# Optimization experiments

Hardware: AMD Instinct MI355X
Metric: run time of the kernel (lower is better)

## Reference

```python
import jax, jax.numpy as jnp
import numpy as np

N = 98304        # total nodes (= 16384 graphs * act_dim 6)
E = 1572864      # edges (avg degree 16)
C = 64           # in_channels
H = 32           # hidden_size
ACT = 6          # act_dim


def setup_inputs() -> dict:
    key = jax.random.key(0)
    ks = jax.random.split(key, 11)
    s = lambda fan: 1.0 / np.sqrt(fan)
    return {
        "state": jax.random.normal(ks[0], (N, C), jnp.float32),
        "edge_index": jax.random.randint(ks[1], (2, E), 0, N, dtype=jnp.int64),
        "conv_W": jax.random.normal(ks[2], (C, C), jnp.float32) * s(C),
        "conv_b": jax.random.normal(ks[3], (C,), jnp.float32) * 0.01,
        "W1": jax.random.normal(ks[4], (C, H), jnp.float32) * s(C),
        "b1": jax.random.normal(ks[5], (H,), jnp.float32) * 0.01,
        "W2": jax.random.normal(ks[6], (H, H), jnp.float32) * s(H),
        "b2": jax.random.normal(ks[7], (H,), jnp.float32) * 0.01,
        "W3": jax.random.normal(ks[8], (H, 1), jnp.float32) * s(H),
        "b3": jax.random.normal(ks[9], (1,), jnp.float32) * 0.01,
    }


def gcn_conv(x, edge_index, W, b):
    # PyG GCNConv: add self-loops, symmetric normalization D^-1/2 (A+I) D^-1/2 (X W) + b
    loops = jnp.arange(N, dtype=edge_index.dtype)
    src = jnp.concatenate([edge_index[0], loops])  # [E+N]
    dst = jnp.concatenate([edge_index[1], loops])  # [E+N]
    deg = jax.ops.segment_sum(jnp.ones(E + N, x.dtype), dst, num_segments=N)
    dinv = jax.lax.rsqrt(deg)                      # deg >= 1 due to self-loops
    norm = dinv[src] * dinv[dst]                   # [E+N]
    h = x @ W                                      # [N, C]
    msg = h[src] * norm[:, None]                   # gather + scale
    return jax.ops.segment_sum(msg, dst, num_segments=N) + b


def reference(state, edge_index, conv_W, conv_b, W1, b1, W2, b2, W3, b3):
    out = jax.nn.relu(gcn_conv(state, edge_index, conv_W, conv_b))
    x = out + state                                # residual
    x = x.reshape(-1, ACT, C)                      # [num_graphs, act_dim, C]
    x = jax.nn.relu(x @ W1 + b1)
    x = jax.nn.relu(x @ W2 + b2)
    x = jax.nn.softplus(x @ W3 + b3)
    concentration = x.squeeze(-1) + 1e-20          # [num_graphs, act_dim]
    return concentration
```

## Files before the change

kernel.cpp:

```cpp
#include <hip/hip_runtime.h>
#include <math.h>

#define Nn 98304
#define Ee 1572864
#define Cc 64
#define Hh 32
#define HB 256
#define EPB (Ee / HB)
#define NST 384
#define SN 256
#define CAP_ST 4800
#define GN 64


__device__ __forceinline__ int detect64(const void* ei) {
    const unsigned int* u = (const unsigned int*)ei;
    int is64 = 1;
    #pragma unroll
    for (int i = 0; i < 16; ++i) is64 &= (u[2 * i + 1] == 0u);
    return is64;
}

__device__ __forceinline__ int load_idx(const void* ei, long e, int is64) {
    if (is64) return (int)((const long long*)ei)[e];
    return ((const int*)ei)[e];
}

__device__ __forceinline__ unsigned short f2bf(float x) {
    union { float f; unsigned int u; } v; v.f = x;
    unsigned int r = v.u + 0x7FFFu + ((v.u >> 16) & 1u);
    return (unsigned short)(r >> 16);
}
__device__ __forceinline__ float bf2f(unsigned short h) {
    union { unsigned int u; float f; } v; v.u = ((unsigned int)h) << 16;
    return v.f;
}

__global__ __launch_bounds__(1024) void k_p1(const void* __restrict__ ei,
                                             unsigned int* __restrict__ aux,
                                             unsigned int* __restrict__ ebuf) {
    __shared__ unsigned int hl[NST];
    __shared__ unsigned int cur[NST];
    int t = threadIdx.x, b = blockIdx.x;
    if (t < NST) hl[t] = 0;
    __syncthreads();
    int is64 = detect64(ei);
    long e0 = (long)b * EPB;
    #pragma unroll
    for (int i = 0; i < EPB / 1024; ++i) {
        int d = load_idx(ei, (long)Ee + e0 + i * 1024 + t, is64);
        atomicAdd(&hl[d >> 8], 1u);
    }
    __syncthreads();
    if (t < NST) cur[t] = hl[t];
    __syncthreads();
    for (int s = 1; s < NST; s <<= 1) {
        unsigned int v = (t < NST && t >= s) ? cur[t - s] : 0u;
        __syncthreads();
        if (t < NST) cur[t] += v;
        __syncthreads();
    }
    if (t < NST) {
        unsigned int ex = cur[t] - hl[t];
        aux[(long)b * NST + t] = ex | (hl[t] << 16);
        cur[t] = ex;
    }
    __syncthreads();
    #pragma unroll
    for (int i = 0; i < EPB / 1024; ++i) {
        long e = e0 + i * 1024 + t;
        int s = load_idx(ei, e, is64);
        int d = load_idx(ei, (long)Ee + e, is64);
        unsigned int pos = atomicAdd(&cur[d >> 8], 1u);
        ebuf[(long)b * EPB + pos] = (unsigned int)s | ((unsigned int)(d & (SN - 1)) << 17);
    }
}

__global__ __launch_bounds__(512) void k_p2(const unsigned int* __restrict__ aux,
                                            const unsigned int* __restrict__ ebuf,
                                            unsigned int* __restrict__ rowOff,
                                            unsigned int* __restrict__ rowEnd,
                                            float* __restrict__ dinv,
                                            unsigned int* __restrict__ srcs) {
    __shared__ unsigned int stage[CAP_ST];
    __shared__ unsigned int rbI[HB];
    __shared__ unsigned int rof[HB];
    __shared__ unsigned int cnt[SN];
    __shared__ unsigned int sc[SN];
    __shared__ unsigned int cur[SN];
    int t = threadIdx.x, st = blockIdx.x;
    if (t < HB) {
        unsigned int av = aux[(long)t * NST + st];
        rof[t] = av & 0xFFFFu;
        rbI[t] = av >> 16;
    }
    if (t < SN) cnt[t] = 0;
    __syncthreads();
    for (int s = 1; s < HB; s <<= 1) {
        unsigned int v = (t < HB && t >= s) ? rbI[t - s] : 0u;
        __syncthreads();
        if (t < HB) rbI[t] += v;
        __syncthreads();
    }
    int total = (int)rbI[HB - 1];
    for (int i = t; i < total; i += 512) {
        int lo = 0, hi = HB - 1;
        while (lo < hi) {
            int mid = (lo + hi) >> 1;
            if (rbI[mid] > (unsigned int)i) hi = mid; else lo = mid + 1;
        }
        unsigned int ex = lo ? rbI[lo - 1] : 0u;
        stage[i] = ebuf[(long)lo * EPB + rof[lo] + ((unsigned int)i - ex)];
    }
    __syncthreads();
    for (int i = t; i < total; i += 512)
        atomicAdd(&cnt[stage[i] >> 17], 1u);
    __syncthreads();
    if (t < SN) sc[t] = cnt[t];
    __syncthreads();
    #pragma unroll
    for (int off = 1; off < SN; off <<= 1) {
        unsigned int v = (t < SN && t >= off) ? sc[t - off] : 0u;
        __syncthreads();
        if (t < SN) sc[t] += v;
        __syncthreads();
    }
    if (t < SN) {
        unsigned int start = (unsigned int)(st * CAP_ST) + sc[t] - cnt[t];
        rowOff[(long)st * SN + t] = start;
        rowEnd[(long)st * SN + t] = start + cnt[t];
        cur[t] = start;
        dinv[(long)st * SN + t] = rsqrtf((float)(cnt[t] + 1));
    }
    __syncthreads();
    for (int i = t; i < total; i += 512) {
        unsigned int u = stage[i];
        unsigned int pos = atomicAdd(&cur[u >> 17], 1u);
        srcs[pos] = u & 0x1FFFFu;
    }
}

__global__ __launch_bounds__(256) void k_gemm(const float* __restrict__ state,
                                              const float* __restrict__ W,
                                              const float* __restrict__ dinv,
                                              unsigned short* __restrict__ gb) {
    __shared__ float Wl[64 * 64];
    __shared__ float Al[64 * 68];
    int t = threadIdx.x;
    long n0 = (long)blockIdx.x * 64;

    const float4* W4 = (const float4*)W;
    float4* Wl4 = (float4*)Wl;
    #pragma unroll
    for (int i = 0; i < 4; ++i) Wl4[i * 256 + t] = W4[i * 256 + t];

    const float4* S4 = (const float4*)(state) + n0 * 16;
    #pragma unroll
    for (int i = 0; i < 4; ++i) {
        int f4 = t + i * 256;
        int r = f4 >> 4, k0 = (f4 & 15) * 4;
        *(float4*)(Al + r * 68 + k0) = S4[f4];
    }
    __syncthreads();

    int r0 = (t >> 4) * 4;
    int c0 = (t & 15) * 4;
    float acc[4][4] = {{0.f}};
    #pragma unroll
    for (int kk = 0; kk < 64; kk += 4) {
        float4 a4[4], w4[4];
        #pragma unroll
        for (int i = 0; i < 4; ++i) a4[i] = *(const float4*)(Al + (r0 + i) * 68 + kk);
        #pragma unroll
        for (int j = 0; j < 4; ++j) w4[j] = *(const float4*)(Wl + (kk + j) * 64 + c0);
        const float* aa = (const float*)a4;
        const float* ww = (const float*)w4;
        #pragma unroll
        for (int i = 0; i < 4; ++i)
            #pragma unroll
            for (int j = 0; j < 4; ++j) {
                float av = aa[i * 4 + j];
                #pragma unroll
                for (int c = 0; c < 4; ++c)
                    acc[i][c] = fmaf(av, ww[j * 4 + c], acc[i][c]);
            }
    }
    #pragma unroll
    for (int i = 0; i < 4; ++i) {
        long n = n0 + r0 + i;
        float dv = dinv[n];
        ushort4 o;
        o.x = f2bf(acc[i][0] * dv); o.y = f2bf(acc[i][1] * dv);
        o.z = f2bf(acc[i][2] * dv); o.w = f2bf(acc[i][3] * dv);
        *(ushort4*)(gb + n * 64 + c0) = o;
    }
}

__global__ __launch_bounds__(512) void k_gf(const unsigned int* __restrict__ rowOff,
                                            const unsigned int* __restrict__ rowEnd,
                                            const unsigned int* __restrict__ srcs,
                                            const unsigned short* __restrict__ gb,
                                            const float* __restrict__ dinv,
                                            const float* __restrict__ state,
                                            const float* __restrict__ conv_b,
                                            const float* __restrict__ W1,
                                            const float* __restrict__ b1,
                                            const float* __restrict__ W2,
                                            const float* __restrict__ b2,
                                            const float* __restrict__ W3,
                                            const float* __restrict__ b3,
                                            float* __restrict__ out) {
    __shared__ float sa[GN * 68];
    __shared__ float hs[GN * 34];
    __shared__ float sW1[Cc * Hh];
    __shared__ float sW2[Hh * Hh];
    __shared__ float sW3[Hh], sb1[Hh], sb2[Hh], scb[Cc];
    __shared__ float sb3;
    int t = threadIdx.x;
    int wave = t >> 6, lane = t & 63;
    long n0 = (long)blockIdx.x * GN;

    for (int i = t; i < Cc * Hh; i += 512) sW1[i] = W1[i];
    for (int i = t; i < Hh * Hh; i += 512) sW2[i] = W2[i];
    if (t < Hh) { sW3[t] = W3[t]; sb1[t] = b1[t]; sb2[t] = b2[t]; }
    if (t >= 64 && t < 128) scb[t - 64] = conv_b[t - 64];
    if (t == 511) sb3 = b3[0];

    {
        int g = lane >> 3;
        int cs = lane & 7;
        int j = wave * 8 + g;
        long n = n0 + j;
        int ptr = (int)rowOff[n];
        int end = (int)rowEnd[n];
        float dv = dinv[n];
        const uint4* gb4 = (const uint4*)gb;

        float a[8];
        {
            uint4 u = gb4[n * 8 + cs];
            union { unsigned int i; float f; } w;
            w.i = u.x << 16;         a[0] = w.f;
            w.i = u.x & 0xFFFF0000u; a[1] = w.f;
            w.i = u.y << 16;         a[2] = w.f;
            w.i = u.y & 0xFFFF0000u; a[3] = w.f;
            w.i = u.z << 16;         a[4] = w.f;
            w.i = u.z & 0xFFFF0000u; a[5] = w.f;
            w.i = u.w << 16;         a[6] = w.f;
            w.i = u.w & 0xFFFF0000u; a[7] = w.f;
        }

        int cnt = end - ptr;
        while (cnt >= 4) {
            int s0 = (int)srcs[ptr];
            int s1 = (int)srcs[ptr + 1];
            int s2 = (int)srcs[ptr + 2];
            int s3 = (int)srcs[ptr + 3];
            uint4 u0 = gb4[(long)s0 * 8 + cs];
            uint4 u1 = gb4[(long)s1 * 8 + cs];
            uint4 u2 = gb4[(long)s2 * 8 + cs];
            uint4 u3 = gb4[(long)s3 * 8 + cs];
            union { unsigned int i; float f; } w;
            w.i = u0.x << 16;         a[0] += w.f;
            w.i = u0.x & 0xFFFF0000u; a[1] += w.f;
            w.i = u0.y << 16;         a[2] += w.f;
            w.i = u0.y & 0xFFFF0000u; a[3] += w.f;
            w.i = u0.z << 16;         a[4] += w.f;
            w.i = u0.z & 0xFFFF0000u; a[5] += w.f;
            w.i = u0.w << 16;         a[6] += w.f;
            w.i = u0.w & 0xFFFF0000u; a[7] += w.f;
            w.i = u1.x << 16;         a[0] += w.f;
            w.i = u1.x & 0xFFFF0000u; a[1] += w.f;
            w.i = u1.y << 16;         a[2] += w.f;
            w.i = u1.y & 0xFFFF0000u; a[3] += w.f;
            w.i = u1.z << 16;         a[4] += w.f;
            w.i = u1.z & 0xFFFF0000u; a[5] += w.f;
            w.i = u1.w << 16;         a[6] += w.f;
            w.i = u1.w & 0xFFFF0000u; a[7] += w.f;
            w.i = u2.x << 16;         a[0] += w.f;
            w.i = u2.x & 0xFFFF0000u; a[1] += w.f;
            w.i = u2.y << 16;         a[2] += w.f;
            w.i = u2.y & 0xFFFF0000u; a[3] += w.f;
            w.i = u2.z << 16;         a[4] += w.f;
            w.i = u2.z & 0xFFFF0000u; a[5] += w.f;
            w.i = u2.w << 16;         a[6] += w.f;
            w.i = u2.w & 0xFFFF0000u; a[7] += w.f;
            w.i = u3.x << 16;         a[0] += w.f;
            w.i = u3.x & 0xFFFF0000u; a[1] += w.f;
            w.i = u3.y << 16;         a[2] += w.f;
            w.i = u3.y & 0xFFFF0000u; a[3] += w.f;
            w.i = u3.z << 16;         a[4] += w.f;
            w.i = u3.z & 0xFFFF0000u; a[5] += w.f;
            w.i = u3.w << 16;         a[6] += w.f;
            w.i = u3.w & 0xFFFF0000u; a[7] += w.f;
            ptr += 4; cnt -= 4;
        }
        while (cnt > 0) {
            int s0 = (int)srcs[ptr];
            uint4 u0 = gb4[(long)s0 * 8 + cs];
            union { unsigned int i; float f; } w;
            w.i = u0.x << 16;         a[0] += w.f;
            w.i = u0.x & 0xFFFF0000u; a[1] += w.f;
            w.i = u0.y << 16;         a[2] += w.f;
            w.i = u0.y & 0xFFFF0000u; a[3] += w.f;
            w.i = u0.z << 16;         a[4] += w.f;
            w.i = u0.z & 0xFFFF0000u; a[5] += w.f;
            w.i = u0.w << 16;         a[6] += w.f;
            w.i = u0.w & 0xFFFF0000u; a[7] += w.f;
            ++ptr; --cnt;
        }

        float* r = sa + j * 68 + cs * 8;
        float4 lo, hi;
        lo.x = a[0] * dv; lo.y = a[1] * dv; lo.z = a[2] * dv; lo.w = a[3] * dv;
        hi.x = a[4] * dv; hi.y = a[5] * dv; hi.z = a[6] * dv; hi.w = a[7] * dv;
        *(float4*)r = lo;
        *(float4*)(r + 4) = hi;
    }
    __syncthreads();

    {
        int j = t >> 3, o = t & 7;
        long n = n0 + j;
        int k0 = o * 8;
        const float4* sp4 = (const float4*)(state + n * 64 + k0);
        float4 s0 = sp4[0], s1 = sp4[1];
        float* r = sa + j * 68 + k0;
        r[0] = fmaxf(r[0] + scb[k0 + 0], 0.f) + s0.x;
        r[1] = fmaxf(r[1] + scb[k0 + 1], 0.f) + s0.y;
        r[2] = fmaxf(r[2] + scb[k0 + 2], 0.f) + s0.z;
        r[3] = fmaxf(r[3] + scb[k0 + 3], 0.f) + s0.w;
        r[4] = fmaxf(r[4] + scb[k0 + 4], 0.f) + s1.x;
        r[5] = fmaxf(r[5] + scb[k0 + 5], 0.f) + s1.y;
        r[6] = fmaxf(r[6] + scb[k0 + 6], 0.f) + s1.z;
        r[7] = fmaxf(r[7] + scb[k0 + 7], 0.f) + s1.w;
    }
    __syncthreads();

    {
        int j = t >> 3, o = t & 7;
        int c0 = o * 4;
        float a0 = sb1[c0], a1 = sb1[c0 + 1], a2 = sb1[c0 + 2], a3 = sb1[c0 + 3];
        #pragma unroll
        for (int k = 0; k < Cc; ++k) {
            float xv = sa[j * 68 + k];
            float4 w = *(const float4*)(sW1 + k * Hh + c0);
            a0 = fmaf(xv, w.x, a0); a1 = fmaf(xv, w.y, a1);
            a2 = fmaf(xv, w.z, a2); a3 = fmaf(xv, w.w, a3);
        }
        float* r = hs + j * 34 + c0;
        r[0] = fmaxf(a0, 0.f); r[1] = fmaxf(a1, 0.f);
        r[2] = fmaxf(a2, 0.f); r[3] = fmaxf(a3, 0.f);
    }
    __syncthreads();

    {
        int j = t >> 3, o = t & 7;
        int c0 = o * 4;
        float a0 = sb2[c0], a1 = sb2[c0 + 1], a2 = sb2[c0 + 2], a3 = sb2[c0 + 3];
        #pragma unroll
        for (int k = 0; k < Hh; ++k) {
            float xv = hs[j * 34 + k];
            float4 w = *(const float4*)(sW2 + k * Hh + c0);
            a0 = fmaf(xv, w.x, a0); a1 = fmaf(xv, w.y, a1);
            a2 = fmaf(xv, w.z, a2); a3 = fmaf(xv, w.w, a3);
        }
        float* r = sa + j * 68 + c0;
        r[0] = fmaxf(a0, 0.f); r[1] = fmaxf(a1, 0.f);
        r[2] = fmaxf(a2, 0.f); r[3] = fmaxf(a3, 0.f);
    }
    __syncthreads();

    if (t < GN) {
        float y = sb3;
        #pragma unroll
        for (int k = 0; k < Hh; ++k) y = fmaf(sa[t * 68 + k], sW3[k], y);
        float sp = fmaxf(y, 0.f) + log1pf(expf(-fabsf(y)));
        out[n0 + t] = sp + 1e-20f;
    }
}

extern "C" void kernel_launch(void* const* d_in, const int* in_sizes, int n_in,
                              void* d_out, int out_size, void* d_ws, size_t ws_size,
                              hipStream_t stream) {
    const float* state  = (const float*)d_in[0];
    const void*  ei     = d_in[1];
    const float* conv_W = (const float*)d_in[2];
    const float* conv_b = (const float*)d_in[3];
    const float* W1 = (const float*)d_in[4];
    const float* b1 = (const float*)d_in[5];
    const float* W2 = (const float*)d_in[6];
    const float* b2 = (const float*)d_in[7];
    const float* W3 = (const float*)d_in[8];
    const float* b3 = (const float*)d_in[9];
    float* out = (float*)d_out;

    float*          dinv   = (float*)d_ws;
    unsigned short* gb     = (unsigned short*)(dinv + Nn);
    unsigned int*   rowOff = (unsigned int*)(gb + (size_t)Nn * 64);
    unsigned int*   rowEnd = rowOff + Nn;
    unsigned int*   aux    = rowEnd + Nn;
    unsigned int*   ebuf   = aux + (size_t)HB * NST;
    unsigned int*   srcs   = ebuf + Ee;

    k_p1<<<HB, 1024, 0, stream>>>(ei, aux, ebuf);
    k_p2<<<NST, 512, 0, stream>>>(aux, ebuf, rowOff, rowEnd, dinv, srcs);
    k_gemm<<<Nn / 64, 256, 0, stream>>>(state, conv_W, dinv, gb);
    k_gf<<<Nn / GN, 512, 0, stream>>>(rowOff, rowEnd, srcs, gb, dinv, state, conv_b,
                                      W1, b1, W2, b2, W3, b3, out);
}
```

Baseline: 174.5 us.

## Software-pipeline neighbor gathers and replace block barriers with wave barriers

The fused aggregation+MLP kernel now issues the next four neighbor-row gathers before accumulating the previous four, so global-load latency overlaps with the bf16 unpack-and-add work. Each wave only touches the eight nodes it owns in shared memory, so the block-wide __syncthreads between MLP stages become wave barriers, plus one block barrier after the weight staging. The final 32-wide dot product is spread across 8 lanes per node with a shuffle reduction instead of 64 serial threads. This keeps more registers live for the prefetched data, and it relies on each wave's shared-memory rows being private to that wave.

After: 172.1 us. No clear change (-1.4%).

```diff
diff --git a/kernel.cpp b/kernel.cpp
--- a/kernel.cpp
+++ b/kernel.cpp
@@ -31,9 +31,28 @@
     unsigned int r = v.u + 0x7FFFu + ((v.u >> 16) & 1u);
     return (unsigned short)(r >> 16);
 }
-__device__ __forceinline__ float bf2f(unsigned short h) {
-    union { unsigned int u; float f; } v; v.u = ((unsigned int)h) << 16;
-    return v.f;
+
+__device__ __forceinline__ void acc_u4(float a[8], uint4 u) {
+    union { unsigned int i; float f; } w;
+    w.i = u.x << 16;         a[0] += w.f;
+    w.i = u.x & 0xFFFF0000u; a[1] += w.f;
+    w.i = u.y << 16;         a[2] += w.f;
+    w.i = u.y & 0xFFFF0000u; a[3] += w.f;
+    w.i = u.z << 16;         a[4] += w.f;
+    w.i = u.z & 0xFFFF0000u; a[5] += w.f;
+    w.i = u.w << 16;         a[6] += w.f;
+    w.i = u.w & 0xFFFF0000u; a[7] += w.f;
+}
+__device__ __forceinline__ void set_u4(float a[8], uint4 u) {
+    union { unsigned int i; float f; } w;
+    w.i = u.x << 16;         a[0] = w.f;
+    w.i = u.x & 0xFFFF0000u; a[1] = w.f;
+    w.i = u.y << 16;         a[2] = w.f;
+    w.i = u.y & 0xFFFF0000u; a[3] = w.f;
+    w.i = u.z << 16;         a[4] = w.f;
+    w.i = u.z & 0xFFFF0000u; a[5] = w.f;
+    w.i = u.w << 16;         a[6] = w.f;
+    w.i = u.w & 0xFFFF0000u; a[7] = w.f;
 }
 
 __global__ __launch_bounds__(1024) void k_p1(const void* __restrict__ ei,
@@ -225,6 +244,7 @@
     if (t < Hh) { sW3[t] = W3[t]; sb1[t] = b1[t]; sb2[t] = b2[t]; }
     if (t >= 64 && t < 128) scb[t - 64] = conv_b[t - 64];
     if (t == 511) sb3 = b3[0];
+    __syncthreads();
 
     {
         int g = lane >> 3;
@@ -237,76 +257,42 @@
         const uint4* gb4 = (const uint4*)gb;
 
         float a[8];
-        {
-            uint4 u = gb4[n * 8 + cs];
-            union { unsigned int i; float f; } w;
-            w.i = u.x << 16;         a[0] = w.f;
-            w.i = u.x & 0xFFFF0000u; a[1] = w.f;
-            w.i = u.y << 16;         a[2] = w.f;
-            w.i = u.y & 0xFFFF0000u; a[3] = w.f;
-            w.i = u.z << 16;         a[4] = w.f;
-            w.i = u.z & 0xFFFF0000u; a[5] = w.f;
-            w.i = u.w << 16;         a[6] = w.f;
-            w.i = u.w & 0xFFFF0000u; a[7] = w.f;
-        }
+        set_u4(a, gb4[n * 8 + cs]);
 
         int cnt = end - ptr;
-        while (cnt >= 4) {
+        uint4 r0, r1, r2, r3;
+        if (cnt >= 4) {
             int s0 = (int)srcs[ptr];
             int s1 = (int)srcs[ptr + 1];
             int s2 = (int)srcs[ptr + 2];
             int s3 = (int)srcs[ptr + 3];
-            uint4 u0 = gb4[(long)s0 * 8 + cs];
-            uint4 u1 = gb4[(long)s1 * 8 + cs];
-            uint4 u2 = gb4[(long)s2 * 8 + cs];
-            uint4 u3 = gb4[(long)s3 * 8 + cs];
-            union { unsigned int i; float f; } w;
-            w.i = u0.x << 16;         a[0] += w.f;
-            w.i = u0.x & 0xFFFF0000u; a[1] += w.f;
-            w.i = u0.y << 16;         a[2] += w.f;
-            w.i = u0.y & 0xFFFF0000u; a[3] += w.f;
-            w.i = u0.z << 16;         a[4] += w.f;
-            w.i = u0.z & 0xFFFF0000u; a[5] += w.f;
-            w.i = u0.w << 16;         a[6] += w.f;
-            w.i = u0.w & 0xFFFF0000u; a[7] += w.f;
-            w.i = u1.x << 16;         a[0] += w.f;
-            w.i = u1.x & 0xFFFF0000u; a[1] += w.f;
-            w.i = u1.y << 16;         a[2] += w.f;
-            w.i = u1.y & 0xFFFF0000u; a[3] += w.f;
-            w.i = u1.z << 16;         a[4] += w.f;
-            w.i = u1.z & 0xFFFF0000u; a[5] += w.f;
-            w.i = u1.w << 16;         a[6] += w.f;
-            w.i = u1.w & 0xFFFF0000u; a[7] += w.f;
-            w.i = u2.x << 16;         a[0] += w.f;
-            w.i = u2.x & 0xFFFF0000u; a[1] += w.f;
-            w.i = u2.y << 16;         a[2] += w.f;
-            w.i = u2.y & 0xFFFF0000u; a[3] += w.f;
-            w.i = u2.z << 16;         a[4] += w.f;
-            w.i = u2.z & 0xFFFF0000u; a[5] += w.f;
-            w.i = u2.w << 16;         a[6] += w.f;
-            w.i = u2.w & 0xFFFF0000u; a[7] += w.f;
-            w.i = u3.x << 16;         a[0] += w.f;
-            w.i = u3.x & 0xFFFF0000u; a[1] += w.f;
-            w.i = u3.y << 16;         a[2] += w.f;
-            w.i = u3.y & 0xFFFF0000u; a[3] += w.f;
-            w.i = u3.z << 16;         a[4] += w.f;
-            w.i = u3.z & 0xFFFF0000u; a[5] += w.f;
-            w.i = u3.w << 16;         a[6] += w.f;
-            w.i = u3.w & 0xFFFF0000u; a[7] += w.f;
+            r0 = gb4[(long)s0 * 8 + cs];
+            r1 = gb4[(long)s1 * 8 + cs];
+            r2 = gb4[(long)s2 * 8 + cs];
+            r3 = gb4[(long)s3 * 8 + cs];
+        }
+        while (cnt >= 8) {
+            int t0 = (int)srcs[ptr + 4];
+            int t1 = (int)srcs[ptr + 5];
+            int t2 = (int)srcs[ptr + 6];
+            int t3 = (int)srcs[ptr + 7];
+            acc_u4(a, r0); acc_u4(a, r1);
+            acc_u4(a, r2); acc_u4(a, r3);
+            r0 = gb4[(long)t0 * 8 + cs];
+            r1 = gb4[(long)t1 * 8 + cs];
+            r2 = gb4[(long)t2 * 8 + cs];
+            r3 = gb4[(long)t3 * 8 + cs];
+            ptr += 4; cnt -= 4;
+        }
+        if (cnt >= 4) {
+            acc_u4(a, r0); acc_u4(a, r1);
+            acc_u4(a, r2); acc_u4(a, r3);
             ptr += 4; cnt -= 4;
         }
         while (cnt > 0) {
             int s0 = (int)srcs[ptr];
             uint4 u0 = gb4[(long)s0 * 8 + cs];
-            union { unsigned int i; float f; } w;
-            w.i = u0.x << 16;         a[0] += w.f;
-            w.i = u0.x & 0xFFFF0000u; a[1] += w.f;
-            w.i = u0.y << 16;         a[2] += w.f;
-            w.i = u0.y & 0xFFFF0000u; a[3] += w.f;
-            w.i = u0.z << 16;         a[4] += w.f;
-            w.i = u0.z & 0xFFFF0000u; a[5] += w.f;
-            w.i = u0.w << 16;         a[6] += w.f;
-            w.i = u0.w & 0xFFFF0000u; a[7] += w.f;
+            acc_u4(a, u0);
             ++ptr; --cnt;
         }
 
@@ -317,7 +303,7 @@
         *(float4*)r = lo;
         *(float4*)(r + 4) = hi;
     }
-    __syncthreads();
+    __builtin_amdgcn_wave_barrier();
 
     {
         int j = t >> 3, o = t & 7;
@@ -335,7 +321,7 @@
         r[6] = fmaxf(r[6] + scb[k0 + 6], 0.f) + s1.z;
         r[7] = fmaxf(r[7] + scb[k0 + 7], 0.f) + s1.w;
     }
-    __syncthreads();
+    __builtin_amdgcn_wave_barrier();
 
     {
         int j = t >> 3, o = t & 7;
@@ -352,7 +338,7 @@
         r[0] = fmaxf(a0, 0.f); r[1] = fmaxf(a1, 0.f);
         r[2] = fmaxf(a2, 0.f); r[3] = fmaxf(a3, 0.f);
     }
-    __syncthreads();
+    __builtin_amdgcn_wave_barrier();
 
     {
         int j = t >> 3, o = t & 7;
@@ -369,14 +355,23 @@
         r[0] = fmaxf(a0, 0.f); r[1] = fmaxf(a1, 0.f);
         r[2] = fmaxf(a2, 0.f); r[3] = fmaxf(a3, 0.f);
     }
-    __syncthreads();
-
-    if (t < GN) {
-        float y = sb3;
-        #pragma unroll
-        for (int k = 0; k < Hh; ++k) y = fmaf(sa[t * 68 + k], sW3[k], y);
-        float sp = fmaxf(y, 0.f) + log1pf(expf(-fabsf(y)));
-        out[n0 + t] = sp + 1e-20f;
+    __builtin_amdgcn_wave_barrier();
+
+    {
+        int g = lane >> 3, o = lane & 7;
+        int j = wave * 8 + g;
+        int k0 = o * 4;
+        float y = 0.f;
+        #pragma unroll
+        for (int k = 0; k < 4; ++k) y = fmaf(sa[j * 68 + k0 + k], sW3[k0 + k], y);
+        y += __shfl_xor(y, 1, 64);
+        y += __shfl_xor(y, 2, 64);
+        y += __shfl_xor(y, 4, 64);
+        if (o == 0) {
+            y += sb3;
+            float sp = fmaxf(y, 0.f) + log1pf(expf(-fabsf(y)));
+            out[n0 + j] = sp + 1e-20f;
+        }
     }
 }
 
```
